# Optimization experiments

Hardware: AMD Instinct MI355X
Metric: run time of the kernel (lower is better)

## Reference

```python
import jax, jax.numpy as jnp
import numpy as np

NUM_HEADS = 16

def setup_inputs() -> dict:
    key = jax.random.key(0)
    ks = jax.random.split(key, 5)
    B, T, C = 2, 2048, 1024
    s = 0.02
    return {
        "x": jax.random.normal(ks[0], (B, T, C), dtype=jnp.float32),
        "in_w": jax.random.normal(ks[1], (3 * C, C), dtype=jnp.float32) * s,
        "in_b": jax.random.normal(ks[2], (3 * C,), dtype=jnp.float32) * s,
        "out_w": jax.random.normal(ks[3], (C, C), dtype=jnp.float32) * s,
        "out_b": jax.random.normal(ks[4], (C,), dtype=jnp.float32) * s,
    }

def reference(x, in_w, in_b, out_w, out_b):
    B, T, C = x.shape
    H = NUM_HEADS
    D = C // H
    qvk = x @ in_w.T + in_b  # (B, T, 3C)
    # einops 'b t (d k h) -> k b h t d': factor 3C as (D, 3, H), D outermost
    qvk = qvk.reshape(B, T, D, 3, H).transpose(3, 0, 4, 1, 2)  # (3, B, H, T, D)
    q, v, k = qvk[0], qvk[1], qvk[2]  # note q, v, k assignment order
    scores = jnp.einsum('bhid,bhjd->bhij', q, k) * (D ** -0.5)  # (B, H, T, T)
    causal = jnp.tril(jnp.ones((T, T), dtype=bool))
    scores = jnp.where(causal, scores, -jnp.inf)
    attn = jax.nn.softmax(scores, axis=-1)
    out = jnp.einsum('bhij,bhjd->bhid', attn, v)  # (B, H, T, D)
    out = out.transpose(0, 2, 1, 3).reshape(B, T, C)  # 'b h t d -> b t (h d)'
    return out @ out_w.T + out_b
```

## Files before the change

kernel.cpp:

```cpp
#include <hip/hip_runtime.h>


#define BB 2
#define TT 2048
#define CC 1024
#define HH 16
#define DD 64
#define MM (BB*TT)
#define N3 (3*CC)
#define BH (BB*HH)

typedef unsigned short u16;
typedef unsigned int   u32;
typedef __bf16 bf16x8 __attribute__((ext_vector_type(8)));
typedef float  f32x4  __attribute__((ext_vector_type(4)));

__device__ __forceinline__ u16 f32_to_bf16(float f) {
  u32 u = __float_as_uint(f);
  return (u16)((u + 0x7fffu + ((u >> 16) & 1u)) >> 16);
}
__device__ __forceinline__ u16 f32_to_bf16_fast(float f) {
  return (u16)((__float_as_uint(f) + 0x8000u) >> 16);
}
__device__ __forceinline__ u32 pack2_bf16(float a, float b) {
  u32 ua = __float_as_uint(a) + 0x8000u;
  u32 ub = __float_as_uint(b) + 0x8000u;
  return __builtin_amdgcn_perm(ub, ua, 0x07060302);
}

__global__ __launch_bounds__(256) void cast_f32_bf16(const float* __restrict__ src,
                                                     u16* __restrict__ dst, int n4) {
  int i = blockIdx.x * 256 + threadIdx.x;
  if (i < n4) {
    float4 f = reinterpret_cast<const float4*>(src)[i];
    uint2 pk;
    pk.x = (u32)f32_to_bf16(f.x) | ((u32)f32_to_bf16(f.y) << 16);
    pk.y = (u32)f32_to_bf16(f.z) | ((u32)f32_to_bf16(f.w) << 16);
    reinterpret_cast<uint2*>(dst)[i] = pk;
  }
}

__device__ __forceinline__ void gemm_core(const u16* __restrict__ Ag,
                                          const u16* __restrict__ Bg,
                                          int K, u16* Al, u16* Bl,
                                          int m0, int n0, f32x4 acc[4][4]) {
  const int tid = threadIdx.x, lane = tid & 63, w = tid >> 6;
  const int quad = lane >> 4, colr = lane & 15;
  const int mw = (w >> 1) * 64, nw = (w & 1) * 64;
  const int srow = lane >> 3, scol = lane & 7;
  const uint4* Al4 = reinterpret_cast<const uint4*>(Al);
  const uint4* Bl4 = reinterpret_cast<const uint4*>(Bl);
  for (int kt = 0; kt < K / 64; ++kt) {
    __syncthreads();
    #pragma unroll
    for (int ii = 0; ii < 4; ++ii) {
      int inst = w * 4 + ii;
      int row = inst * 8 + srow;
      int cs = scol ^ (row & 7);
      const u16* ga = Ag + (size_t)(m0 + row) * K + kt * 64 + cs * 8;
      const u16* gb = Bg + (size_t)(n0 + row) * K + kt * 64 + cs * 8;
      __builtin_amdgcn_global_load_lds(
          (const __attribute__((address_space(1))) void*)ga,
          (__attribute__((address_space(3))) void*)(Al + inst * 512), 16, 0, 0);
      __builtin_amdgcn_global_load_lds(
          (const __attribute__((address_space(1))) void*)gb,
          (__attribute__((address_space(3))) void*)(Bl + inst * 512), 16, 0, 0);
    }
    __syncthreads();
    #pragma unroll
    for (int ks = 0; ks < 2; ++ks) {
      bf16x8 af[4], bfr[4];
      #pragma unroll
      for (int t = 0; t < 4; ++t) {
        int mrow = mw + t * 16 + colr;
        af[t]  = __builtin_bit_cast(bf16x8, Al4[mrow * 8 + ((ks * 4 + quad) ^ (mrow & 7))]);
        int nrow = nw + t * 16 + colr;
        bfr[t] = __builtin_bit_cast(bf16x8, Bl4[nrow * 8 + ((ks * 4 + quad) ^ (nrow & 7))]);
      }
      #pragma unroll
      for (int mt = 0; mt < 4; ++mt)
        #pragma unroll
        for (int nt = 0; nt < 4; ++nt)
          acc[mt][nt] = __builtin_amdgcn_mfma_f32_16x16x32_bf16(af[mt], bfr[nt], acc[mt][nt], 0, 0, 0);
    }
  }
}

__global__ __launch_bounds__(256) void gemm_qkv(const u16* __restrict__ xb,
                                                const u16* __restrict__ wb,
                                                const float* __restrict__ in_b,
                                                u16* __restrict__ Y) {
  __shared__ __align__(16) u16 Al[128 * 64];
  __shared__ __align__(16) u16 Bl[128 * 64];
  const int lane = threadIdx.x & 63, w = threadIdx.x >> 6;
  const int quad = lane >> 4, colr = lane & 15;
  const int mw = (w >> 1) * 64, nw = (w & 1) * 64;
  const int m0 = blockIdx.x * 128, n0 = blockIdx.y * 128;
  f32x4 acc[4][4];
  #pragma unroll
  for (int mt = 0; mt < 4; ++mt)
    #pragma unroll
    for (int nt = 0; nt < 4; ++nt) acc[mt][nt] = (f32x4){0.f, 0.f, 0.f, 0.f};
  gemm_core(xb, wb, CC, Al, Bl, m0, n0, acc);
  float bias[4];
  #pragma unroll
  for (int nt = 0; nt < 4; ++nt) bias[nt] = in_b[n0 + nw + nt * 16 + colr];
  #pragma unroll
  for (int mt = 0; mt < 4; ++mt)
    #pragma unroll
    for (int e = 0; e < 4; ++e) {
      int row = m0 + mw + mt * 16 + quad * 4 + e;
      #pragma unroll
      for (int nt = 0; nt < 4; ++nt)
        Y[(size_t)row * N3 + n0 + nw + nt * 16 + colr] = f32_to_bf16(acc[mt][nt][e] + bias[nt]);
    }
}

__global__ __launch_bounds__(256) void repack_qkv(const u16* __restrict__ Y,
                                                  u16* __restrict__ qkv) {
  __shared__ __align__(16) u16 Yl[N3];
  const int m = blockIdx.x, tid = threadIdx.x;
  const int b_ = m >> 11, t = m & (TT - 1);
  const uint4* Yg = reinterpret_cast<const uint4*>(Y + (size_t)m * N3);
  uint4* Yl4 = reinterpret_cast<uint4*>(Yl);
  for (int i = tid; i < N3 / 8; i += 256) Yl4[i] = Yg[i];
  __syncthreads();
  for (int it = tid; it < 768; it += 256) {
    int h = it & 15, s = (it >> 4) % 3, dg = it / 48;
    int col = s * 16 + h;
    u32 lo = (u32)Yl[(dg * 4 + 0) * 48 + col] | ((u32)Yl[(dg * 4 + 1) * 48 + col] << 16);
    u32 hi = (u32)Yl[(dg * 4 + 2) * 48 + col] | ((u32)Yl[(dg * 4 + 3) * 48 + col] << 16);
    uint2 pk; pk.x = lo; pk.y = hi;
    size_t base = (((size_t)s * BH + b_ * HH + h) * TT + t) * DD + dg * 4;
    *reinterpret_cast<uint2*>(qkv + base) = pk;
  }
}

__global__ __launch_bounds__(256) void attn_mfma(const u16* __restrict__ qkv,
                                                 u16* __restrict__ aout) {
  __shared__ __align__(16) u32   Vt[64 * 36];
  __shared__ __align__(16) float Pl[4 * 32 * 68];
  const int tid  = threadIdx.x;
  const int lane = tid & 63, w = tid >> 6;
  const int quad = lane >> 4, colr = lane & 15;
  const int flat = blockIdx.x;
  const int bh = (flat & 7) * 4 + (flat >> 6);
  const int pr = (flat >> 3) & 7;
  const int b_ = bh >> 4, h = bh & 15;

  const uint4* Qg4 = reinterpret_cast<const uint4*>(qkv + (size_t)bh * TT * DD);
  const uint4* Vg4 = reinterpret_cast<const uint4*>(qkv + ((size_t)BH + bh) * TT * DD);
  const uint4* Kg4 = reinterpret_cast<const uint4*>(qkv + ((size_t)2 * BH + bh) * TT * DD);
  const uint4*  Vt4 = reinterpret_cast<const uint4*>(Vt);
  const float4* Pl4 = reinterpret_cast<const float4*>(Pl);

  const int s_jp = tid & 31, s_oct = tid >> 5;
  const int wbase = w * (32 * 68);

  for (int pass = 0; pass < 2; ++pass) {
    const int qt = pass ? (15 - pr) : pr;
    const int i0 = qt * 128;
    const int jmax = 2 * qt + 1;

    bf16x8 qa[2][2];
    #pragma unroll
    for (int u = 0; u < 2; ++u)
      #pragma unroll
      for (int ks = 0; ks < 2; ++ks)
        qa[u][ks] = __builtin_bit_cast(bf16x8,
            Qg4[(size_t)(i0 + w * 32 + u * 16 + colr) * 8 + ks * 4 + quad]);

    f32x4 oacc[2][4];
    #pragma unroll
    for (int u = 0; u < 2; ++u)
      #pragma unroll
      for (int dt = 0; dt < 4; ++dt) oacc[u][dt] = (f32x4){0.f, 0.f, 0.f, 0.f};
    float lp[2] = {0.f, 0.f};

    uint4 va = Vg4[(size_t)(2 * s_jp) * 8 + s_oct];
    uint4 vb = Vg4[(size_t)(2 * s_jp + 1) * 8 + s_oct];

    for (int jt = 0; jt <= jmax; ++jt) {
      const int j0 = jt * 64;
      uint4 kraw[4][2];
      #pragma unroll
      for (int t4 = 0; t4 < 4; ++t4)
        #pragma unroll
        for (int ks = 0; ks < 2; ++ks)
          kraw[t4][ks] = Kg4[(size_t)(j0 + t4 * 16 + colr) * 8 + ks * 4 + quad];

      __syncthreads();
      {
        u32 aw[4] = {va.x, va.y, va.z, va.w};
        u32 bw[4] = {vb.x, vb.y, vb.z, vb.w};
        #pragma unroll
        for (int m = 0; m < 4; ++m) {
          Vt[(s_oct * 8 + 2 * m)     * 36 + s_jp] = __builtin_amdgcn_perm(bw[m], aw[m], 0x05040100);
          Vt[(s_oct * 8 + 2 * m + 1) * 36 + s_jp] = __builtin_amdgcn_perm(bw[m], aw[m], 0x07060302);
        }
      }
      __syncthreads();
      if (jt < jmax) {
        int nj = j0 + 64;
        va = Vg4[(size_t)(nj + 2 * s_jp) * 8 + s_oct];
        vb = Vg4[(size_t)(nj + 2 * s_jp + 1) * 8 + s_oct];
      }

      f32x4 sacc[2][4];
      #pragma unroll
      for (int u = 0; u < 2; ++u)
        #pragma unroll
        for (int t4 = 0; t4 < 4; ++t4) sacc[u][t4] = (f32x4){0.f, 0.f, 0.f, 0.f};
      #pragma unroll
      for (int t4 = 0; t4 < 4; ++t4)
        #pragma unroll
        for (int ks = 0; ks < 2; ++ks) {
          bf16x8 kb = __builtin_bit_cast(bf16x8, kraw[t4][ks]);
          #pragma unroll
          for (int u = 0; u < 2; ++u)
            sacc[u][t4] = __builtin_amdgcn_mfma_f32_16x16x32_bf16(qa[u][ks], kb, sacc[u][t4], 0, 0, 0);
        }

      const bool maskt = (jt >= 2 * qt);
      const int joff = (jt - 2 * qt) * 64;
      #pragma unroll
      for (int u = 0; u < 2; ++u)
        #pragma unroll
        for (int t4 = 0; t4 < 4; ++t4)
          #pragma unroll
          for (int rg = 0; rg < 4; ++rg) {
            float p = __builtin_amdgcn_exp2f(sacc[u][t4][rg] * 0.18033688011112042f);
            if (maskt && (joff + t4 * 16 + colr > w * 32 + u * 16 + quad * 4 + rg)) p = 0.f;
            Pl[wbase + (u * 16 + quad * 4 + rg) * 68 + t4 * 16 + colr] = p;
          }

      bf16x8 pa[2][2];
      #pragma unroll
      for (int u = 0; u < 2; ++u)
        #pragma unroll
        for (int ks = 0; ks < 2; ++ks) {
          int b4 = (wbase + (u * 16 + colr) * 68 + ks * 32 + quad * 8) >> 2;
          float4 f0 = Pl4[b4], f1 = Pl4[b4 + 1];
          lp[u] += ((f0.x + f0.y) + (f0.z + f0.w)) + ((f1.x + f1.y) + (f1.z + f1.w));
          uint4 up;
          up.x = pack2_bf16(f0.x, f0.y); up.y = pack2_bf16(f0.z, f0.w);
          up.z = pack2_bf16(f1.x, f1.y); up.w = pack2_bf16(f1.z, f1.w);
          pa[u][ks] = __builtin_bit_cast(bf16x8, up);
        }

      #pragma unroll
      for (int dt = 0; dt < 4; ++dt)
        #pragma unroll
        for (int ks = 0; ks < 2; ++ks) {
          bf16x8 vfr = __builtin_bit_cast(bf16x8, Vt4[(dt * 16 + colr) * 9 + ks * 4 + quad]);
          #pragma unroll
          for (int u = 0; u < 2; ++u)
            oacc[u][dt] = __builtin_amdgcn_mfma_f32_16x16x32_bf16(pa[u][ks], vfr, oacc[u][dt], 0, 0, 0);
        }
    }

    #pragma unroll
    for (int u = 0; u < 2; ++u) {
      float ls = lp[u];
      ls += __shfl_xor(ls, 16);
      ls += __shfl_xor(ls, 32);
      float linv[4];
      #pragma unroll
      for (int rg = 0; rg < 4; ++rg)
        linv[rg] = 1.0f / __shfl(ls, quad * 4 + rg);
      #pragma unroll
      for (int dt = 0; dt < 4; ++dt)
        #pragma unroll
        for (int rg = 0; rg < 4; ++rg) {
          int ig = i0 + w * 32 + u * 16 + quad * 4 + rg;
          size_t off = ((size_t)(b_ * TT + ig)) * CC + h * DD + dt * 16 + colr;
          aout[off] = f32_to_bf16_fast(oacc[u][dt][rg] * linv[rg]);
        }
    }
  }
}

__global__ __launch_bounds__(256) void gemm_out(const u16* __restrict__ ab,
                                                const u16* __restrict__ owb,
                                                const float* __restrict__ out_b,
                                                float* __restrict__ out) {
  __shared__ __align__(16) u16 Al[128 * 64];
  __shared__ __align__(16) u16 Bl[128 * 64];
  const int lane = threadIdx.x & 63, w = threadIdx.x >> 6;
  const int quad = lane >> 4, colr = lane & 15;
  const int mw = (w >> 1) * 64, nw = (w & 1) * 64;
  const int m0 = blockIdx.x * 128, n0 = blockIdx.y * 128;
  f32x4 acc[4][4];
  #pragma unroll
  for (int mt = 0; mt < 4; ++mt)
    #pragma unroll
    for (int nt = 0; nt < 4; ++nt) acc[mt][nt] = (f32x4){0.f, 0.f, 0.f, 0.f};
  gemm_core(ab, owb, CC, Al, Bl, m0, n0, acc);
  float bias[4];
  #pragma unroll
  for (int nt = 0; nt < 4; ++nt) bias[nt] = out_b[n0 + nw + nt * 16 + colr];
  #pragma unroll
  for (int mt = 0; mt < 4; ++mt)
    #pragma unroll
    for (int e = 0; e < 4; ++e) {
      int row = m0 + mw + mt * 16 + quad * 4 + e;
      #pragma unroll
      for (int nt = 0; nt < 4; ++nt)
        out[(size_t)row * CC + n0 + nw + nt * 16 + colr] = acc[mt][nt][e] + bias[nt];
    }
}

extern "C" void kernel_launch(void* const* d_in, const int* in_sizes, int n_in,
                              void* d_out, int out_size, void* d_ws, size_t ws_size,
                              hipStream_t stream) {
  const float* x     = (const float*)d_in[0];
  const float* in_w  = (const float*)d_in[1];
  const float* in_b  = (const float*)d_in[2];
  const float* out_w = (const float*)d_in[3];
  const float* out_b = (const float*)d_in[4];
  float* out = (float*)d_out;

  char* ws = (char*)d_ws;
  u16* xb  = (u16*)(ws + 0);
  u16* ab  = (u16*)(ws + 0);
  u16* wb  = (u16*)(ws + 8388608);
  u16* owb = (u16*)(ws + 14680064);
  u16* Y   = (u16*)(ws + 16777216);
  u16* qkv = (u16*)(ws + 41943040);

  cast_f32_bf16<<<dim3(MM * CC / 4 / 256), 256, 0, stream>>>(x, xb, MM * CC / 4);
  cast_f32_bf16<<<dim3(N3 * CC / 4 / 256), 256, 0, stream>>>(in_w, wb, N3 * CC / 4);
  cast_f32_bf16<<<dim3(CC * CC / 4 / 256), 256, 0, stream>>>(out_w, owb, CC * CC / 4);

  gemm_qkv<<<dim3(MM / 128, N3 / 128), 256, 0, stream>>>(xb, wb, in_b, Y);
  repack_qkv<<<dim3(MM), 256, 0, stream>>>(Y, qkv);
  attn_mfma<<<dim3(256), 256, 0, stream>>>(qkv, ab);
  gemm_out<<<dim3(MM / 128, CC / 128), 256, 0, stream>>>(ab, owb, out_b, out);
}
```

Before: 231.5 us.

## Merge cast kernels and use 8 waves with double-buffered V in attention

The three f32-to-bf16 cast launches become one combined kernel that picks its source buffer by index range, which removes two launches. The attention kernel moves from 4 waves of 32 query rows to 8 waves of 16 rows (512 threads). V tiles are now double-buffered in shared memory, so one __syncthreads per key tile is dropped, and only half the threads stage V. This gives more waves per CU for latency hiding, at the cost of each wave redoing the K loads, half the MFMA reuse per K fragment, and higher shared memory use.

```diff
diff --git a/kernel.cpp b/kernel.cpp
--- a/kernel.cpp
+++ b/kernel.cpp
@@ -28,16 +28,25 @@
   return __builtin_amdgcn_perm(ub, ua, 0x07060302);
 }
 
-__global__ __launch_bounds__(256) void cast_f32_bf16(const float* __restrict__ src,
-                                                     u16* __restrict__ dst, int n4) {
+#define N4_X  (MM * CC / 4)
+#define N4_W  (N3 * CC / 4)
+#define N4_OW (CC * CC / 4)
+__global__ __launch_bounds__(256) void cast_all(const float* __restrict__ x,
+                                                const float* __restrict__ in_w,
+                                                const float* __restrict__ out_w,
+                                                u16* __restrict__ xb,
+                                                u16* __restrict__ wb,
+                                                u16* __restrict__ owb) {
   int i = blockIdx.x * 256 + threadIdx.x;
-  if (i < n4) {
-    float4 f = reinterpret_cast<const float4*>(src)[i];
-    uint2 pk;
-    pk.x = (u32)f32_to_bf16(f.x) | ((u32)f32_to_bf16(f.y) << 16);
-    pk.y = (u32)f32_to_bf16(f.z) | ((u32)f32_to_bf16(f.w) << 16);
-    reinterpret_cast<uint2*>(dst)[i] = pk;
-  }
+  const float* src; u16* dst; int j;
+  if (i < N4_X)            { src = x;     dst = xb;  j = i; }
+  else if (i < N4_X + N4_W){ src = in_w;  dst = wb;  j = i - N4_X; }
+  else                     { src = out_w; dst = owb; j = i - N4_X - N4_W; }
+  float4 f = reinterpret_cast<const float4*>(src)[j];
+  uint2 pk;
+  pk.x = (u32)f32_to_bf16(f.x) | ((u32)f32_to_bf16(f.y) << 16);
+  pk.y = (u32)f32_to_bf16(f.z) | ((u32)f32_to_bf16(f.w) << 16);
+  reinterpret_cast<uint2*>(dst)[j] = pk;
 }
 
 __device__ __forceinline__ void gemm_core(const u16* __restrict__ Ag,
@@ -136,10 +145,10 @@
   }
 }
 
-__global__ __launch_bounds__(256) void attn_mfma(const u16* __restrict__ qkv,
+__global__ __launch_bounds__(512) void attn_mfma(const u16* __restrict__ qkv,
                                                  u16* __restrict__ aout) {
-  __shared__ __align__(16) u32   Vt[64 * 36];
-  __shared__ __align__(16) float Pl[4 * 32 * 68];
+  __shared__ __align__(16) u32   Vt[2][64 * 36];
+  __shared__ __align__(16) float Pl[8 * 16 * 68];
   const int tid  = threadIdx.x;
   const int lane = tid & 63, w = tid >> 6;
   const int quad = lane >> 4, colr = lane & 15;
@@ -151,37 +160,39 @@
   const uint4* Qg4 = reinterpret_cast<const uint4*>(qkv + (size_t)bh * TT * DD);
   const uint4* Vg4 = reinterpret_cast<const uint4*>(qkv + ((size_t)BH + bh) * TT * DD);
   const uint4* Kg4 = reinterpret_cast<const uint4*>(qkv + ((size_t)2 * BH + bh) * TT * DD);
-  const uint4*  Vt4 = reinterpret_cast<const uint4*>(Vt);
   const float4* Pl4 = reinterpret_cast<const float4*>(Pl);
 
-  const int s_jp = tid & 31, s_oct = tid >> 5;
-  const int wbase = w * (32 * 68);
+  const int s_jp = tid & 31, s_oct = (tid >> 5) & 7;
+  const bool stager = (tid < 256);
+  const int wbase = w * (16 * 68);
 
   for (int pass = 0; pass < 2; ++pass) {
     const int qt = pass ? (15 - pr) : pr;
     const int i0 = qt * 128;
     const int jmax = 2 * qt + 1;
 
-    bf16x8 qa[2][2];
-    #pragma unroll
-    for (int u = 0; u < 2; ++u)
-      #pragma unroll
-      for (int ks = 0; ks < 2; ++ks)
-        qa[u][ks] = __builtin_bit_cast(bf16x8,
-            Qg4[(size_t)(i0 + w * 32 + u * 16 + colr) * 8 + ks * 4 + quad]);
-
-    f32x4 oacc[2][4];
-    #pragma unroll
-    for (int u = 0; u < 2; ++u)
-      #pragma unroll
-      for (int dt = 0; dt < 4; ++dt) oacc[u][dt] = (f32x4){0.f, 0.f, 0.f, 0.f};
-    float lp[2] = {0.f, 0.f};
-
-    uint4 va = Vg4[(size_t)(2 * s_jp) * 8 + s_oct];
-    uint4 vb = Vg4[(size_t)(2 * s_jp + 1) * 8 + s_oct];
+    bf16x8 qa[2];
+    #pragma unroll
+    for (int ks = 0; ks < 2; ++ks)
+      qa[ks] = __builtin_bit_cast(bf16x8,
+          Qg4[(size_t)(i0 + w * 16 + colr) * 8 + ks * 4 + quad]);
+
+    f32x4 oacc[4];
+    #pragma unroll
+    for (int dt = 0; dt < 4; ++dt) oacc[dt] = (f32x4){0.f, 0.f, 0.f, 0.f};
+    float lp = 0.f;
+
+    uint4 va, vb;
+    if (stager) {
+      va = Vg4[(size_t)(2 * s_jp) * 8 + s_oct];
+      vb = Vg4[(size_t)(2 * s_jp + 1) * 8 + s_oct];
+    }
 
     for (int jt = 0; jt <= jmax; ++jt) {
       const int j0 = jt * 64;
+      u32* vtw = Vt[jt & 1];
+      const uint4* vt4 = reinterpret_cast<const uint4*>(Vt[jt & 1]);
+
       uint4 kraw[4][2];
       #pragma unroll
       for (int t4 = 0; t4 < 4; ++t4)
@@ -189,94 +200,81 @@
         for (int ks = 0; ks < 2; ++ks)
           kraw[t4][ks] = Kg4[(size_t)(j0 + t4 * 16 + colr) * 8 + ks * 4 + quad];
 
-      __syncthreads();
-      {
+      if (stager) {
         u32 aw[4] = {va.x, va.y, va.z, va.w};
         u32 bw[4] = {vb.x, vb.y, vb.z, vb.w};
         #pragma unroll
         for (int m = 0; m < 4; ++m) {
-          Vt[(s_oct * 8 + 2 * m)     * 36 + s_jp] = __builtin_amdgcn_perm(bw[m], aw[m], 0x05040100);
-          Vt[(s_oct * 8 + 2 * m + 1) * 36 + s_jp] = __builtin_amdgcn_perm(bw[m], aw[m], 0x07060302);
+          vtw[(s_oct * 8 + 2 * m)     * 36 + s_jp] = __builtin_amdgcn_perm(bw[m], aw[m], 0x05040100);
+          vtw[(s_oct * 8 + 2 * m + 1) * 36 + s_jp] = __builtin_amdgcn_perm(bw[m], aw[m], 0x07060302);
+        }
+        if (jt < jmax) {
+          int nj = j0 + 64;
+          va = Vg4[(size_t)(nj + 2 * s_jp) * 8 + s_oct];
+          vb = Vg4[(size_t)(nj + 2 * s_jp + 1) * 8 + s_oct];
         }
       }
       __syncthreads();
-      if (jt < jmax) {
-        int nj = j0 + 64;
-        va = Vg4[(size_t)(nj + 2 * s_jp) * 8 + s_oct];
-        vb = Vg4[(size_t)(nj + 2 * s_jp + 1) * 8 + s_oct];
-      }
-
-      f32x4 sacc[2][4];
-      #pragma unroll
-      for (int u = 0; u < 2; ++u)
-        #pragma unroll
-        for (int t4 = 0; t4 < 4; ++t4) sacc[u][t4] = (f32x4){0.f, 0.f, 0.f, 0.f};
+
+      f32x4 sacc[4];
+      #pragma unroll
+      for (int t4 = 0; t4 < 4; ++t4) sacc[t4] = (f32x4){0.f, 0.f, 0.f, 0.f};
       #pragma unroll
       for (int t4 = 0; t4 < 4; ++t4)
         #pragma unroll
         for (int ks = 0; ks < 2; ++ks) {
           bf16x8 kb = __builtin_bit_cast(bf16x8, kraw[t4][ks]);
-          #pragma unroll
-          for (int u = 0; u < 2; ++u)
-            sacc[u][t4] = __builtin_amdgcn_mfma_f32_16x16x32_bf16(qa[u][ks], kb, sacc[u][t4], 0, 0, 0);
+          sacc[t4] = __builtin_amdgcn_mfma_f32_16x16x32_bf16(qa[ks], kb, sacc[t4], 0, 0, 0);
         }
 
       const bool maskt = (jt >= 2 * qt);
       const int joff = (jt - 2 * qt) * 64;
       #pragma unroll
-      for (int u = 0; u < 2; ++u)
-        #pragma unroll
-        for (int t4 = 0; t4 < 4; ++t4)
-          #pragma unroll
-          for (int rg = 0; rg < 4; ++rg) {
-            float p = __builtin_amdgcn_exp2f(sacc[u][t4][rg] * 0.18033688011112042f);
-            if (maskt && (joff + t4 * 16 + colr > w * 32 + u * 16 + quad * 4 + rg)) p = 0.f;
-            Pl[wbase + (u * 16 + quad * 4 + rg) * 68 + t4 * 16 + colr] = p;
-          }
-
-      bf16x8 pa[2][2];
-      #pragma unroll
-      for (int u = 0; u < 2; ++u)
+      for (int t4 = 0; t4 < 4; ++t4)
+        #pragma unroll
+        for (int rg = 0; rg < 4; ++rg) {
+          float p = __builtin_amdgcn_exp2f(sacc[t4][rg] * 0.18033688011112042f);
+          if (maskt && (joff + t4 * 16 + colr > w * 16 + quad * 4 + rg)) p = 0.f;
+          Pl[wbase + (quad * 4 + rg) * 68 + t4 * 16 + colr] = p;
+        }
+
+      bf16x8 pa[2];
+      #pragma unroll
+      for (int ks = 0; ks < 2; ++ks) {
+        int b4 = (wbase + colr * 68 + ks * 32 + quad * 8) >> 2;
+        float4 f0 = Pl4[b4], f1 = Pl4[b4 + 1];
+        lp += ((f0.x + f0.y) + (f0.z + f0.w)) + ((f1.x + f1.y) + (f1.z + f1.w));
+        uint4 up;
+        up.x = pack2_bf16(f0.x, f0.y); up.y = pack2_bf16(f0.z, f0.w);
+        up.z = pack2_bf16(f1.x, f1.y); up.w = pack2_bf16(f1.z, f1.w);
+        pa[ks] = __builtin_bit_cast(bf16x8, up);
+      }
+
+      #pragma unroll
+      for (int dt = 0; dt < 4; ++dt)
         #pragma unroll
         for (int ks = 0; ks < 2; ++ks) {
-          int b4 = (wbase + (u * 16 + colr) * 68 + ks * 32 + quad * 8) >> 2;
-          float4 f0 = Pl4[b4], f1 = Pl4[b4 + 1];
-          lp[u] += ((f0.x + f0.y) + (f0.z + f0.w)) + ((f1.x + f1.y) + (f1.z + f1.w));
-          uint4 up;
-          up.x = pack2_bf16(f0.x, f0.y); up.y = pack2_bf16(f0.z, f0.w);
-          up.z = pack2_bf16(f1.x, f1.y); up.w = pack2_bf16(f1.z, f1.w);
-          pa[u][ks] = __builtin_bit_cast(bf16x8, up);
-        }
-
-      #pragma unroll
-      for (int dt = 0; dt < 4; ++dt)
-        #pragma unroll
-        for (int ks = 0; ks < 2; ++ks) {
-          bf16x8 vfr = __builtin_bit_cast(bf16x8, Vt4[(dt * 16 + colr) * 9 + ks * 4 + quad]);
-          #pragma unroll
-          for (int u = 0; u < 2; ++u)
-            oacc[u][dt] = __builtin_amdgcn_mfma_f32_16x16x32_bf16(pa[u][ks], vfr, oacc[u][dt], 0, 0, 0);
-        }
-    }
-
-    #pragma unroll
-    for (int u = 0; u < 2; ++u) {
-      float ls = lp[u];
-      ls += __shfl_xor(ls, 16);
-      ls += __shfl_xor(ls, 32);
-      float linv[4];
-      #pragma unroll
-      for (int rg = 0; rg < 4; ++rg)
-        linv[rg] = 1.0f / __shfl(ls, quad * 4 + rg);
-      #pragma unroll
-      for (int dt = 0; dt < 4; ++dt)
-        #pragma unroll
-        for (int rg = 0; rg < 4; ++rg) {
-          int ig = i0 + w * 32 + u * 16 + quad * 4 + rg;
-          size_t off = ((size_t)(b_ * TT + ig)) * CC + h * DD + dt * 16 + colr;
-          aout[off] = f32_to_bf16_fast(oacc[u][dt][rg] * linv[rg]);
-        }
-    }
+          bf16x8 vfr = __builtin_bit_cast(bf16x8, vt4[(dt * 16 + colr) * 9 + ks * 4 + quad]);
+          oacc[dt] = __builtin_amdgcn_mfma_f32_16x16x32_bf16(pa[ks], vfr, oacc[dt], 0, 0, 0);
+        }
+    }
+
+    float ls = lp;
+    ls += __shfl_xor(ls, 16);
+    ls += __shfl_xor(ls, 32);
+    float linv[4];
+    #pragma unroll
+    for (int rg = 0; rg < 4; ++rg)
+      linv[rg] = 1.0f / __shfl(ls, quad * 4 + rg);
+    #pragma unroll
+    for (int dt = 0; dt < 4; ++dt)
+      #pragma unroll
+      for (int rg = 0; rg < 4; ++rg) {
+        int ig = i0 + w * 16 + quad * 4 + rg;
+        size_t off = ((size_t)(b_ * TT + ig)) * CC + h * DD + dt * 16 + colr;
+        aout[off] = f32_to_bf16_fast(oacc[dt][rg] * linv[rg]);
+      }
+    __syncthreads();
   }
 }
 
@@ -328,12 +326,10 @@
   u16* Y   = (u16*)(ws + 16777216);
   u16* qkv = (u16*)(ws + 41943040);
 
-  cast_f32_bf16<<<dim3(MM * CC / 4 / 256), 256, 0, stream>>>(x, xb, MM * CC / 4);
-  cast_f32_bf16<<<dim3(N3 * CC / 4 / 256), 256, 0, stream>>>(in_w, wb, N3 * CC / 4);
-  cast_f32_bf16<<<dim3(CC * CC / 4 / 256), 256, 0, stream>>>(out_w, owb, CC * CC / 4);
+  cast_all<<<dim3((N4_X + N4_W + N4_OW) / 256), 256, 0, stream>>>(x, in_w, out_w, xb, wb, owb);
 
   gemm_qkv<<<dim3(MM / 128, N3 / 128), 256, 0, stream>>>(xb, wb, in_b, Y);
   repack_qkv<<<dim3(MM), 256, 0, stream>>>(Y, qkv);
-  attn_mfma<<<dim3(256), 256, 0, stream>>>(qkv, ab);
+  attn_mfma<<<dim3(256), 512, 0, stream>>>(qkv, ab);
   gemm_out<<<dim3(MM / 128, CC / 128), 256, 0, stream>>>(ab, owb, out_b, out);
 }
```

After: 249.6 us. 7.8% more time.
